# Optimization experiments

Hardware: AMD Instinct MI355X
Metric: run time of the kernel (lower is better)

Reference implementation:

```python
import jax, jax.numpy as jnp
import numpy as np

NO_EDGE_OFFSET_T_NORM = 10.0
NO_EDGE_OFFSET_T_CONORM = -10.0

B, I, O = 64, 1024, 1024  # num_samples, in_features, out_features
N_EDGE_TYPES = 3          # 0=no_edge, 1=edge (identity), 2=negation (1-x)
N_OP_TYPES = 2            # 0=T_Norm.min, 1=T_Conorm.max


def setup_inputs() -> dict:
    key = jax.random.key(0)
    k1, k2, k3, k4 = jax.random.split(key, 4)
    # fuzzy inputs in [0, 1]
    x = jax.random.uniform(k1, (B, I), dtype=jnp.float32)
    # operator_type_counts is all-ones -> uniform multinomial over operator types (per node)
    op_idx = jax.random.randint(k2, (O,), 0, N_OP_TYPES, dtype=jnp.int32)
    # edge_type_count is all-ones -> uniform multinomial over edge types,
    # resampled per (sample, node, edge) exactly as the double python loop does
    et = jax.random.randint(k3, (B, O, I), 0, N_EDGE_TYPES, dtype=jnp.int32)
    # source fix-up: if every sampled index is 0 (all no_edge), force one random edge to type 1
    all_zero = jnp.all(et == 0, axis=-1)                      # [B, O]
    rand_pos = jax.random.randint(k4, (B, O), 0, I, dtype=jnp.int32)
    force = all_zero[:, :, None] & (jnp.arange(I)[None, None, :] == rand_pos[:, :, None])
    et = jnp.where(force, 1, et)
    return {"x": x, "edge_type_idx": et, "op_idx": op_idx}


def reference(x, edge_type_idx, op_idx):
    # x: [B, I] float; edge_type_idx: [B, O, I] int; op_idx: [O] int
    is_tnorm = (op_idx == 0)                                   # [O], op 0 = min (T_Norm)
    xb = x[:, None, :]                                         # [B, 1, I]
    # edge value: identity for edge/no_edge, 1-x for negation
    vals = jnp.where(edge_type_idx == 2, 1.0 - xb, xb)         # [B, O, I]
    # no_edge offset: +10 under t-norm (ignored by min), -10 under t-conorm (ignored by max)
    offset = jnp.where(is_tnorm[None, :, None], NO_EDGE_OFFSET_T_NORM, NO_EDGE_OFFSET_T_CONORM)
    vals = vals + jnp.where(edge_type_idx == 0, offset, 0.0)
    tn = jnp.min(vals, axis=-1)                                # [B, O] t-norm (min)
    tc = jnp.max(vals, axis=-1)                                # [B, O] t-conorm (max)
    return jnp.where(is_tnorm[None, :], tn, tc)
```

## Files before the change

### kernel.cpp

```cpp
#include <hip/hip_runtime.h>


constexpr int B = 64;
constexpr int I = 1024;
constexpr int O = 1024;
constexpr int ROWS_PER_BLOCK = 4;

__global__ __launch_bounds__(256) void ffcl_kernel(
    const float* __restrict__ x,
    const int*   __restrict__ et,
    const int*   __restrict__ op,
    float*       __restrict__ out)
{
    __shared__ float xs[I];

    const int t   = threadIdx.x;
    const int r0  = blockIdx.x * ROWS_PER_BLOCK;
    const int b   = r0 >> 10;

    {
        const float4* src = reinterpret_cast<const float4*>(x + (size_t)b * I);
        reinterpret_cast<float4*>(xs)[t] = src[t];
    }
    __syncthreads();

    const int wid  = t >> 6;
    const int lane = t & 63;
    const int r    = r0 + wid;
    const int o    = r & (O - 1);

    const bool  is_t = (op[o] == 0);
    const float sgn  = is_t ? -1.0f : 1.0f;
    const float off  = is_t ? 10.0f : -10.0f;

    const int4* etp = reinterpret_cast<const int4*>(et + (size_t)r * I);

    float acc = -3.0e38f;
    #pragma unroll
    for (int j = 0; j < 4; ++j) {
        const int col = j * 256 + lane * 4;
        const int4  e  = etp[col >> 2];
        const float4 xv = *reinterpret_cast<const float4*>(&xs[col]);

        float v;
        v = (e.x == 2) ? 1.0f - xv.x : xv.x;  v += (e.x == 0) ? off : 0.0f;  acc = fmaxf(acc, sgn * v);
        v = (e.y == 2) ? 1.0f - xv.y : xv.y;  v += (e.y == 0) ? off : 0.0f;  acc = fmaxf(acc, sgn * v);
        v = (e.z == 2) ? 1.0f - xv.z : xv.z;  v += (e.z == 0) ? off : 0.0f;  acc = fmaxf(acc, sgn * v);
        v = (e.w == 2) ? 1.0f - xv.w : xv.w;  v += (e.w == 0) ? off : 0.0f;  acc = fmaxf(acc, sgn * v);
    }

    #pragma unroll
    for (int s = 32; s > 0; s >>= 1)
        acc = fmaxf(acc, __shfl_xor(acc, s, 64));

    if (lane == 0)
        out[r] = sgn * acc;
}

extern "C" void kernel_launch(void* const* d_in, const int* in_sizes, int n_in,
                              void* d_out, int out_size, void* d_ws, size_t ws_size,
                              hipStream_t stream) {
    const float* x  = (const float*)d_in[0];
    const int*   et = (const int*)d_in[1];
    const int*   op = (const int*)d_in[2];
    float*       out = (float*)d_out;

    const int n_rows = B * O;
    const int grid   = n_rows / ROWS_PER_BLOCK;
    ffcl_kernel<<<grid, 256, 0, stream>>>(x, et, op, out);
}
```

Measured before the change: 352.5 us.

## Process eight rows per wave with double-buffered register prefetch of edge types

Each wavefront now handles eight consecutive output rows instead of one. It keeps the x slice in registers rather than shared memory and software-pipelines the edge-type loads with two register buffers, so the next row's loads are in flight while the current row is reduced. The block-level shared-memory staging and barrier are removed. The aim is more memory-level parallelism on the bandwidth-bound stream, at the cost of higher register pressure and fewer blocks in the grid.

```diff
diff --git a/kernel.cpp b/kernel.cpp
--- a/kernel.cpp
+++ b/kernel.cpp
@@ -4,7 +4,11 @@
 constexpr int B = 64;
 constexpr int I = 1024;
 constexpr int O = 1024;
-constexpr int ROWS_PER_BLOCK = 4;
+constexpr int ROWS_PER_WAVE = 8;
+constexpr int BLOCKS = (B * O) / (ROWS_PER_WAVE * 4);
+
+typedef int   iv4 __attribute__((ext_vector_type(4)));
+typedef float fv4 __attribute__((ext_vector_type(4)));
 
 __global__ __launch_bounds__(256) void ffcl_kernel(
     const float* __restrict__ x,
@@ -12,60 +16,82 @@
     const int*   __restrict__ op,
     float*       __restrict__ out)
 {
-    __shared__ float xs[I];
-
-    const int t   = threadIdx.x;
-    const int r0  = blockIdx.x * ROWS_PER_BLOCK;
-    const int b   = r0 >> 10;
-
-    {
-        const float4* src = reinterpret_cast<const float4*>(x + (size_t)b * I);
-        reinterpret_cast<float4*>(xs)[t] = src[t];
-    }
-    __syncthreads();
-
+    const int t    = threadIdx.x;
     const int wid  = t >> 6;
     const int lane = t & 63;
-    const int r    = r0 + wid;
-    const int o    = r & (O - 1);
+    const int wave = blockIdx.x * 4 + wid;
+    const int r_base = wave * ROWS_PER_WAVE;
+    const int b      = r_base >> 10;
+    const int o_base = r_base & (O - 1);
 
-    const bool  is_t = (op[o] == 0);
-    const float sgn  = is_t ? -1.0f : 1.0f;
-    const float off  = is_t ? 10.0f : -10.0f;
+    fv4 xv[4];
+    #pragma unroll
+    for (int j = 0; j < 4; ++j)
+        xv[j] = *reinterpret_cast<const fv4*>(x + (size_t)b * I + j * 256 + lane * 4);
 
-    const int4* etp = reinterpret_cast<const int4*>(et + (size_t)r * I);
-
-    float acc = -3.0e38f;
+    float sgn[ROWS_PER_WAVE], off[ROWS_PER_WAVE];
     #pragma unroll
-    for (int j = 0; j < 4; ++j) {
-        const int col = j * 256 + lane * 4;
-        const int4  e  = etp[col >> 2];
-        const float4 xv = *reinterpret_cast<const float4*>(&xs[col]);
-
-        float v;
-        v = (e.x == 2) ? 1.0f - xv.x : xv.x;  v += (e.x == 0) ? off : 0.0f;  acc = fmaxf(acc, sgn * v);
-        v = (e.y == 2) ? 1.0f - xv.y : xv.y;  v += (e.y == 0) ? off : 0.0f;  acc = fmaxf(acc, sgn * v);
-        v = (e.z == 2) ? 1.0f - xv.z : xv.z;  v += (e.z == 0) ? off : 0.0f;  acc = fmaxf(acc, sgn * v);
-        v = (e.w == 2) ? 1.0f - xv.w : xv.w;  v += (e.w == 0) ? off : 0.0f;  acc = fmaxf(acc, sgn * v);
+    for (int rr = 0; rr < ROWS_PER_WAVE; ++rr) {
+        const bool is_t = (op[o_base + rr] == 0);
+        sgn[rr] = is_t ? -1.0f : 1.0f;
+        off[rr] = is_t ? 10.0f : -10.0f;
     }
 
+    const iv4* pe = reinterpret_cast<const iv4*>(et + (size_t)r_base * I) + lane;
+
+    float acc[ROWS_PER_WAVE];
     #pragma unroll
-    for (int s = 32; s > 0; s >>= 1)
-        acc = fmaxf(acc, __shfl_xor(acc, s, 64));
+    for (int rr = 0; rr < ROWS_PER_WAVE; ++rr) acc[rr] = -3.0e38f;
 
-    if (lane == 0)
-        out[r] = sgn * acc;
+    iv4 eA[4], eB[4];
+
+#define PREFETCH(BUF, RR) { \
+    _Pragma("unroll") \
+    for (int j = 0; j < 4; ++j) BUF[j] = pe[(RR) * 256 + j * 64]; }
+
+#define CONSUME(E, RR) { \
+    _Pragma("unroll") \
+    for (int j = 0; j < 4; ++j) { \
+        float v; \
+        v = (E[j].x == 2) ? 1.0f - xv[j].x : xv[j].x;  v += (E[j].x == 0) ? off[RR] : 0.0f;  acc[RR] = fmaxf(acc[RR], sgn[RR] * v); \
+        v = (E[j].y == 2) ? 1.0f - xv[j].y : xv[j].y;  v += (E[j].y == 0) ? off[RR] : 0.0f;  acc[RR] = fmaxf(acc[RR], sgn[RR] * v); \
+        v = (E[j].z == 2) ? 1.0f - xv[j].z : xv[j].z;  v += (E[j].z == 0) ? off[RR] : 0.0f;  acc[RR] = fmaxf(acc[RR], sgn[RR] * v); \
+        v = (E[j].w == 2) ? 1.0f - xv[j].w : xv[j].w;  v += (E[j].w == 0) ? off[RR] : 0.0f;  acc[RR] = fmaxf(acc[RR], sgn[RR] * v); \
+    } }
+
+    PREFETCH(eA, 0)
+    PREFETCH(eB, 1)  CONSUME(eA, 0)
+    PREFETCH(eA, 2)  CONSUME(eB, 1)
+    PREFETCH(eB, 3)  CONSUME(eA, 2)
+    PREFETCH(eA, 4)  CONSUME(eB, 3)
+    PREFETCH(eB, 5)  CONSUME(eA, 4)
+    PREFETCH(eA, 6)  CONSUME(eB, 5)
+    PREFETCH(eB, 7)  CONSUME(eA, 6)
+                     CONSUME(eB, 7)
+
+#undef PREFETCH
+#undef CONSUME
+
+    float keep = 0.0f;
+    #pragma unroll
+    for (int rr = 0; rr < ROWS_PER_WAVE; ++rr) {
+        float a = acc[rr];
+        #pragma unroll
+        for (int s = 32; s > 0; s >>= 1)
+            a = fmaxf(a, __shfl_xor(a, s, 64));
+        if (lane == rr) keep = sgn[rr] * a;
+    }
+    if (lane < ROWS_PER_WAVE)
+        out[r_base + lane] = keep;
 }
 
 extern "C" void kernel_launch(void* const* d_in, const int* in_sizes, int n_in,
                               void* d_out, int out_size, void* d_ws, size_t ws_size,
                               hipStream_t stream) {
-    const float* x  = (const float*)d_in[0];
-    const int*   et = (const int*)d_in[1];
-    const int*   op = (const int*)d_in[2];
+    const float* x   = (const float*)d_in[0];
+    const int*   et  = (const int*)d_in[1];
+    const int*   op  = (const int*)d_in[2];
     float*       out = (float*)d_out;
 
-    const int n_rows = B * O;
-    const int grid   = n_rows / ROWS_PER_BLOCK;
-    ffcl_kernel<<<grid, 256, 0, stream>>>(x, et, op, out);
+    ffcl_kernel<<<BLOCKS, 256, 0, stream>>>(x, et, op, out);
 }
```

Result: no change. 357.2 us (+1.3%).
